# Kernel optimization log

Measured on AMD Instinct MI355X. Metric: run time of the kernel, lower is better.

## Reference

```python
import jax, jax.numpy as jnp
import numpy as np

T, B, V, E, H, K = 256, 512, 50000, 300, 100, 8


def _lstm_dir(x, wih, whh, bih, bhh, reverse):
    # x: [T,B,D]; wih: [4H,D]; whh: [4H,H]. PyTorch gate order: i,f,g,o.
    xp = jnp.einsum('tbd,gd->tbg', x, wih) + bih + bhh  # precompute input projections
    h0 = jnp.zeros((x.shape[1], whh.shape[1]), x.dtype)
    c0 = jnp.zeros_like(h0)

    def step(carry, xt):
        h, c = carry
        g = xt + h @ whh.T
        i, f, gg, o = jnp.split(g, 4, axis=-1)
        i = jax.nn.sigmoid(i); f = jax.nn.sigmoid(f)
        gg = jnp.tanh(gg); o = jax.nn.sigmoid(o)
        c = f * c + i * gg
        h = o * jnp.tanh(c)
        return (h, c), h

    _, hs = jax.lax.scan(step, (h0, c0), xp, reverse=reverse)
    return hs  # [T,B,H]


def _bilstm(x, pf, pb):
    hf = _lstm_dir(x, *pf, reverse=False)
    hb = _lstm_dir(x, *pb, reverse=True)
    return jnp.concatenate([hf, hb], axis=-1)  # [T,B,2H]


def _crf_llh(em, tags, maskf, start_t, end_t, trans):
    # torchcrf log-likelihood, reduction='sum'. em: [T,B,K], tags/maskf: [T,B]
    barange = jnp.arange(em.shape[1])
    # numerator: score of gold path
    num = start_t[tags[0]] + em[0, barange, tags[0]]
    trans_sc = trans[tags[:-1], tags[1:]]                                   # [T-1,B]
    em_sc = jnp.take_along_axis(em[1:], tags[1:, :, None], axis=2)[..., 0]  # [T-1,B]
    num = num + jnp.sum((trans_sc + em_sc) * maskf[1:], axis=0)
    seq_ends = maskf.sum(0).astype(jnp.int32) - 1
    num = num + end_t[tags[seq_ends, barange]]
    # denominator: forward algorithm (log partition)
    score0 = start_t + em[0]  # [B,K]

    def step(score, inp):
        em_t, m_t = inp
        nxt = jax.scipy.special.logsumexp(score[:, :, None] + trans[None], axis=1) + em_t
        return jnp.where(m_t[:, None] > 0, nxt, score), None

    scoreT, _ = jax.lax.scan(step, score0, (em[1:], maskf[1:]))
    denom = jax.scipy.special.logsumexp(scoreT + end_t, axis=1)
    return jnp.sum(num - denom)


def _viterbi(em, start_t, end_t, trans):
    # mask is all ones -> fixed-length decode. em: [T,B,K] -> tags [T,B]
    score0 = start_t + em[0]

    def step(score, em_t):
        br = score[:, :, None] + trans            # [B,K,K]
        idx = jnp.argmax(br, axis=1)              # [B,K] backpointers
        return jnp.max(br, axis=1) + em_t, idx

    scoreT, hist = jax.lax.scan(step, score0, em[1:])  # hist: [T-1,B,K]
    last = jnp.argmax(scoreT + end_t, axis=1)          # [B]
    barange = jnp.arange(em.shape[1])

    def back(nxt, h):
        prev = h[barange, nxt]
        return prev, prev

    _, prevs = jax.lax.scan(back, last, hist, reverse=True)  # [T-1,B]
    return jnp.concatenate([prevs, last[None]], axis=0)      # [T,B]


def setup_inputs() -> dict:
    key = jax.random.key(0)
    ks = jax.random.split(key, 32)
    u = lambda k, shape, s: jax.random.uniform(k, shape, jnp.float32, -s, s)
    kl = 1.0 / np.sqrt(H)
    inp = {
        'sentence': jax.random.randint(ks[0], (T, B), 0, V, dtype=jnp.int32),
        'tags': jax.random.randint(ks[1], (T, B), 0, K, dtype=jnp.int32),
        'mask': jnp.ones((T, B), dtype=bool),
        'emb': jax.random.normal(ks[2], (V, E), jnp.float32),
        # layer 0 (input dim E)
        'wih0f': u(ks[3], (4 * H, E), kl), 'whh0f': u(ks[4], (4 * H, H), kl),
        'bih0f': u(ks[5], (4 * H,), kl), 'bhh0f': u(ks[6], (4 * H,), kl),
        'wih0b': u(ks[7], (4 * H, E), kl), 'whh0b': u(ks[8], (4 * H, H), kl),
        'bih0b': u(ks[9], (4 * H,), kl), 'bhh0b': u(ks[10], (4 * H,), kl),
        # layer 1 (input dim 2H)
        'wih1f': u(ks[11], (4 * H, 2 * H), kl), 'whh1f': u(ks[12], (4 * H, H), kl),
        'bih1f': u(ks[13], (4 * H,), kl), 'bhh1f': u(ks[14], (4 * H,), kl),
        'wih1b': u(ks[15], (4 * H, 2 * H), kl), 'whh1b': u(ks[16], (4 * H, H), kl),
        'bih1b': u(ks[17], (4 * H,), kl), 'bhh1b': u(ks[18], (4 * H,), kl),
        # linear 2H -> K
        'wl': u(ks[19], (K, 2 * H), 1.0 / np.sqrt(2 * H)), 'bl': u(ks[20], (K,), 1.0 / np.sqrt(2 * H)),
        # CRF params (torchcrf init: uniform(-0.1, 0.1))
        'start_t': u(ks[21], (K,), 0.1), 'end_t': u(ks[22], (K,), 0.1),
        'trans': u(ks[23], (K, K), 0.1),
    }
    return inp


def reference(sentence, tags, mask, emb,
              wih0f, whh0f, bih0f, bhh0f, wih0b, whh0b, bih0b, bhh0b,
              wih1f, whh1f, bih1f, bhh1f, wih1b, whh1b, bih1b, bhh1b,
              wl, bl, start_t, end_t, trans):
    x = emb[sentence]                                        # [T,B,E]
    h1 = _bilstm(x, (wih0f, whh0f, bih0f, bhh0f), (wih0b, whh0b, bih0b, bhh0b))
    h2 = _bilstm(h1, (wih1f, whh1f, bih1f, bhh1f), (wih1b, whh1b, bih1b, bhh1b))
    em = jnp.einsum('tbh,kh->tbk', h2, wl) + bl              # emissions [T,B,K]
    maskf = mask.astype(em.dtype)
    loss = _crf_llh(em, tags, maskf, start_t, end_t, trans)
    decode = _viterbi(em, start_t, end_t, trans)
    return loss, decode
```

## Files before the change

kernel.cpp:

```cpp
#include <hip/hip_runtime.h>
#include <math.h>


#define T_LEN 256
#define B_SZ  512
#define TCH   32

__device__ __forceinline__ float sigm(float x) { return 1.f / (1.f + __expf(-x)); }
__device__ __forceinline__ float tanh_f(float x) {
  float e = __expf(-2.f * fabsf(x));
  float r = (1.f - e) / (1.f + e);
  return copysignf(r, x);
}

__global__ __launch_bounds__(256) void pack_kernel(
    const float* __restrict__ wih0f, const float* __restrict__ bih0f, const float* __restrict__ bhh0f,
    const float* __restrict__ wih0b, const float* __restrict__ bih0b, const float* __restrict__ bhh0b,
    const float* __restrict__ wih1f, const float* __restrict__ bih1f, const float* __restrict__ bhh1f,
    const float* __restrict__ wih1b, const float* __restrict__ bih1b, const float* __restrict__ bhh1b,
    float* __restrict__ W0, float* __restrict__ B0,
    float* __restrict__ W1, float* __restrict__ B1,
    float* __restrict__ out0) {
  int idx = blockIdx.x * blockDim.x + threadIdx.x;
  int stride = gridDim.x * blockDim.x;
  if (idx == 0) out0[0] = 0.f;
  for (int i = idx; i < 800 * 300; i += stride) {
    int g = i / 300, d = i - g * 300;
    W0[i] = (g < 400) ? wih0f[g * 300 + d] : wih0b[(g - 400) * 300 + d];
  }
  for (int i = idx; i < 800 * 200; i += stride) {
    int g = i / 200, d = i - g * 200;
    W1[i] = (g < 400) ? wih1f[g * 200 + d] : wih1b[(g - 400) * 200 + d];
  }
  for (int i = idx; i < 800; i += stride) {
    B0[i] = (i < 400) ? (bih0f[i] + bhh0f[i]) : (bih0b[i - 400] + bhh0b[i - 400]);
    B1[i] = (i < 400) ? (bih1f[i] + bhh1f[i]) : (bih1b[i - 400] + bhh1b[i - 400]);
  }
}

#define BM 128
#define BN 128
#define BK 16
__device__ __forceinline__ void gemm_body(
    const float* __restrict__ A, const float* __restrict__ W,
    const float* __restrict__ bias, float* __restrict__ C,
    int M, int N, int Kd, int m0, int n0,
    float (*As)[BM], float (*Ws)[BN]) {
  const int tid = threadIdx.x;
  const int tx = tid & 15, ty = tid >> 4;
  const int lm = tid & 127;
  const int lk = (tid >> 7) * 8;

  float acc[8][8];
  float bj[8];
#pragma unroll
  for (int j = 0; j < 8; ++j) {
    int n = n0 + tx * 8 + j;
    bj[j] = (n < N) ? bias[n] : 0.f;
  }
#pragma unroll
  for (int i = 0; i < 8; ++i)
#pragma unroll
    for (int j = 0; j < 8; ++j) acc[i][j] = bj[j];

  float4 av0, av1, wv0, wv1;
  av0 = av1 = wv0 = wv1 = make_float4(0.f, 0.f, 0.f, 0.f);
  {
    if (m0 + lm < M && lk < Kd)
      av0 = *(const float4*)(A + (size_t)(m0 + lm) * Kd + lk);
    if (m0 + lm < M && lk + 4 < Kd)
      av1 = *(const float4*)(A + (size_t)(m0 + lm) * Kd + lk + 4);
    if (n0 + lm < N && lk < Kd)
      wv0 = *(const float4*)(W + (size_t)(n0 + lm) * Kd + lk);
    if (n0 + lm < N && lk + 4 < Kd)
      wv1 = *(const float4*)(W + (size_t)(n0 + lm) * Kd + lk + 4);
  }

  for (int k0 = 0; k0 < Kd; k0 += BK) {
    __syncthreads();
    As[lk + 0][lm] = av0.x; As[lk + 1][lm] = av0.y;
    As[lk + 2][lm] = av0.z; As[lk + 3][lm] = av0.w;
    As[lk + 4][lm] = av1.x; As[lk + 5][lm] = av1.y;
    As[lk + 6][lm] = av1.z; As[lk + 7][lm] = av1.w;
    Ws[lk + 0][lm] = wv0.x; Ws[lk + 1][lm] = wv0.y;
    Ws[lk + 2][lm] = wv0.z; Ws[lk + 3][lm] = wv0.w;
    Ws[lk + 4][lm] = wv1.x; Ws[lk + 5][lm] = wv1.y;
    Ws[lk + 6][lm] = wv1.z; Ws[lk + 7][lm] = wv1.w;
    __syncthreads();
    int k0n = k0 + BK;
    av0 = av1 = wv0 = wv1 = make_float4(0.f, 0.f, 0.f, 0.f);
    if (k0n < Kd) {
      if (m0 + lm < M && k0n + lk < Kd)
        av0 = *(const float4*)(A + (size_t)(m0 + lm) * Kd + k0n + lk);
      if (m0 + lm < M && k0n + lk + 4 < Kd)
        av1 = *(const float4*)(A + (size_t)(m0 + lm) * Kd + k0n + lk + 4);
      if (n0 + lm < N && k0n + lk < Kd)
        wv0 = *(const float4*)(W + (size_t)(n0 + lm) * Kd + k0n + lk);
      if (n0 + lm < N && k0n + lk + 4 < Kd)
        wv1 = *(const float4*)(W + (size_t)(n0 + lm) * Kd + k0n + lk + 4);
    }
#pragma unroll
    for (int kk = 0; kk < BK; ++kk) {
      float a[8], w[8];
      *(float4*)&a[0] = *(const float4*)&As[kk][ty * 8];
      *(float4*)&a[4] = *(const float4*)&As[kk][ty * 8 + 4];
      *(float4*)&w[0] = *(const float4*)&Ws[kk][tx * 8];
      *(float4*)&w[4] = *(const float4*)&Ws[kk][tx * 8 + 4];
#pragma unroll
      for (int i = 0; i < 8; ++i)
#pragma unroll
        for (int j = 0; j < 8; ++j) acc[i][j] += a[i] * w[j];
    }
  }
#pragma unroll
  for (int i = 0; i < 8; ++i) {
    int m = m0 + ty * 8 + i;
    if (m < M) {
#pragma unroll
      for (int j0 = 0; j0 < 8; j0 += 4) {
        int n = n0 + tx * 8 + j0;
        if (n < N) {
          float4 o = make_float4(acc[i][j0], acc[i][j0 + 1], acc[i][j0 + 2], acc[i][j0 + 3]);
          *(float4*)(C + (size_t)m * N + n) = o;
        }
      }
    }
  }
}

__global__ __launch_bounds__(256, 2) void gemm_tn(
    const float* __restrict__ A, const float* __restrict__ W,
    const float* __restrict__ bias, float* __restrict__ C,
    int M, int N, int Kd) {
  __shared__ float As[BK][BM];
  __shared__ float Ws[BK][BN];
  gemm_body(A, W, bias, C, M, N, Kd, blockIdx.x * BM, blockIdx.y * BN, As, Ws);
}

__global__ __launch_bounds__(256, 2) void gemm_dual(
    const float* __restrict__ h1, const float* __restrict__ W1,
    const float* __restrict__ B1, float* __restrict__ XPF,
    float* __restrict__ XPB, int baseF, int baseB, int B) {
  __shared__ float As[BK][BM];
  __shared__ float Ws[BK][BN];
  const int dir = blockIdx.z;
  const float* A = h1 + (size_t)(dir ? baseB : baseF) * B * 200;
  const float* W = W1 + (size_t)dir * 80000;
  const float* bias = B1 + dir * 400;
  float* C = dir ? XPB : XPF;
  gemm_body(A, W, bias, C, TCH * B, 400, 200, blockIdx.x * BM, blockIdx.y * BN, As, Ws);
}

__global__ __launch_bounds__(256, 2) void lstm2(
    const float* __restrict__ XPf, const float* __restrict__ XPb,
    int xp_stride,
    const int* __restrict__ gather,
    const float* __restrict__ whhF, const float* __restrict__ whhB,
    float* __restrict__ stateH, float* __restrict__ stateC,
    float* __restrict__ hout,
    int tbaseF, int tbaseB, int TC, int first, int B) {
  const int tid = threadIdx.x;
  const int j = tid >> 1;
  const int gp = tid & 1;
  const bool act = (j < 100);
  const int bpd = B >> 1;
  const int dir = (blockIdx.x >= (unsigned)bpd) ? 1 : 0;
  const int b0 = (dir ? (blockIdx.x - bpd) : blockIdx.x) * 2;
  const float* __restrict__ XP = dir ? XPb : XPf;
  const float* __restrict__ whh = dir ? whhB : whhF;
  const int tbase = dir ? tbaseB : tbaseF;
  const int tstep = dir ? -1 : 1;
  const int tfirst = dir ? (tbase + TC - 1) : tbase;
  const int cg0 = gp * 200 + j;
  const int cg1 = cg0 + 100;

  __shared__ float h_s[2][2][100];

  float4 w0[25], w1[25];
  {
    const float* p0 = whh + (size_t)(2 * gp) * 10000 + (size_t)j * 100;
    if (act) {
#pragma unroll
      for (int q = 0; q < 25; ++q) {
        w0[q] = *(const float4*)(p0 + q * 4);
        w1[q] = *(const float4*)(p0 + 10000 + q * 4);
      }
    } else {
#pragma unroll
      for (int q = 0; q < 25; ++q) {
        w0[q] = make_float4(0.f, 0.f, 0.f, 0.f);
        w1[q] = make_float4(0.f, 0.f, 0.f, 0.f);
      }
    }
  }

  float c0v = 0.f, c1v = 0.f;
  if (gp == 0 && act) {
    if (!first) {
      c0v = stateC[((size_t)dir * B + b0 + 0) * 100 + j];
      c1v = stateC[((size_t)dir * B + b0 + 1) * 100 + j];
      h_s[0][0][j] = stateH[((size_t)dir * B + b0 + 0) * 100 + j];
      h_s[0][1][j] = stateH[((size_t)dir * B + b0 + 1) * 100 + j];
    } else {
      h_s[0][0][j] = 0.f;
      h_s[0][1][j] = 0.f;
    }
  }

  auto rowptr = [&](int tt, int bb) -> const float* {
    size_t r = gather ? (size_t)gather[(size_t)tt * B + b0 + bb]
                      : (size_t)(tt - tbase) * B + b0 + bb;
    return XP + r * (size_t)xp_stride;
  };

  float x00 = 0.f, x01 = 0.f, x10 = 0.f, x11 = 0.f;
  {
    const float* r0 = rowptr(tfirst, 0);
    const float* r1 = rowptr(tfirst, 1);
    if (act) { x00 = r0[cg0]; x10 = r0[cg1]; x01 = r1[cg0]; x11 = r1[cg1]; }
  }
  const float* baseN0 = XP;
  const float* baseN1 = XP;
  if (TC > 1) { baseN0 = rowptr(tfirst + tstep, 0); baseN1 = rowptr(tfirst + tstep, 1); }

  __syncthreads();

  int cur = 0;
  for (int s = 0; s < TC; ++s) {
    const int t = tfirst + s * tstep;
    float nx00 = 0.f, nx01 = 0.f, nx10 = 0.f, nx11 = 0.f;
    if (act && s + 1 < TC) {
      nx00 = baseN0[cg0]; nx10 = baseN0[cg1];
      nx01 = baseN1[cg0]; nx11 = baseN1[cg1];
    }
    if (s + 2 < TC) {
      baseN0 = rowptr(t + 2 * tstep, 0);
      baseN1 = rowptr(t + 2 * tstep, 1);
    }
    float a00 = 0.f, a01 = 0.f, a10 = 0.f, a11 = 0.f;
    const float* hb0 = h_s[cur][0];
    const float* hb1 = h_s[cur][1];
#pragma unroll
    for (int q = 0; q < 25; ++q) {
      float4 h0 = *(const float4*)(hb0 + q * 4);
      float4 h1v = *(const float4*)(hb1 + q * 4);
      float4 W0q = w0[q], W1q = w1[q];
      a00 += W0q.x * h0.x + W0q.y * h0.y + W0q.z * h0.z + W0q.w * h0.w;
      a10 += W1q.x * h0.x + W1q.y * h0.y + W1q.z * h0.z + W1q.w * h0.w;
      a01 += W0q.x * h1v.x + W0q.y * h1v.y + W0q.z * h1v.z + W0q.w * h1v.w;
      a11 += W1q.x * h1v.x + W1q.y * h1v.y + W1q.z * h1v.z + W1q.w * h1v.w;
    }
    a00 += x00; a10 += x10; a01 += x01; a11 += x11;
    float g0 = __shfl_xor(a00, 1);
    float g1 = __shfl_xor(a01, 1);
    float o0 = __shfl_xor(a10, 1);
    float o1 = __shfl_xor(a11, 1);
    const int nxt = cur ^ 1;
    if (gp == 0 && act) {
      float i0 = sigm(a00), f0 = sigm(a10);
      c0v = f0 * c0v + i0 * tanh_f(g0);
      float h0n = sigm(o0) * tanh_f(c0v);
      float i1 = sigm(a01), f1 = sigm(a11);
      c1v = f1 * c1v + i1 * tanh_f(g1);
      float h1n = sigm(o1) * tanh_f(c1v);
      h_s[nxt][0][j] = h0n;
      h_s[nxt][1][j] = h1n;
      hout[((size_t)t * B + b0 + 0) * 200 + dir * 100 + j] = h0n;
      hout[((size_t)t * B + b0 + 1) * 200 + dir * 100 + j] = h1n;
    }
    __syncthreads();
    cur = nxt;
    x00 = nx00; x01 = nx01; x10 = nx10; x11 = nx11;
  }
  if (gp == 0 && act) {
    stateH[((size_t)dir * B + b0 + 0) * 100 + j] = h_s[cur][0][j];
    stateH[((size_t)dir * B + b0 + 1) * 100 + j] = h_s[cur][1][j];
    stateC[((size_t)dir * B + b0 + 0) * 100 + j] = c0v;
    stateC[((size_t)dir * B + b0 + 1) * 100 + j] = c1v;
  }
}

__global__ __launch_bounds__(256) void em_kernel(
    const float* __restrict__ h2, const float* __restrict__ wl,
    const float* __restrict__ bl_, float* __restrict__ em) {
  __shared__ float hsb[32][200];
  __shared__ float wls[8 * 200];
  __shared__ float bls[8];
  const int tid = threadIdx.x;
  const int row0 = blockIdx.x * 32;
  for (int i = tid; i < 1600; i += 256) wls[i] = wl[i];
  if (tid < 8) bls[tid] = bl_[tid];
  for (int i = tid; i < 1600; i += 256) {
    int r = i / 50, q = i - r * 50;
    *(float4*)&hsb[r][q * 4] = *(const float4*)(h2 + (size_t)(row0 + r) * 200 + q * 4);
  }
  __syncthreads();
  const int r_l = tid >> 3, k = tid & 7;
  float acc = bls[k];
#pragma unroll
  for (int d4 = 0; d4 < 50; ++d4) {
    float4 h = *(const float4*)&hsb[r_l][d4 * 4];
    float4 wv = *(const float4*)&wls[k * 200 + d4 * 4];
    acc += h.x * wv.x + h.y * wv.y + h.z * wv.z + h.w * wv.w;
  }
  em[(size_t)(row0 + r_l) * 8 + k] = acc;
}

__global__ __launch_bounds__(64) void crf_kernel(
    const float* __restrict__ em, const int* __restrict__ tags,
    const float* __restrict__ start_t, const float* __restrict__ end_t,
    const float* __restrict__ trans, float* __restrict__ loss_out,
    int T, int B) {
  const int tid = threadIdx.x;
  const int bl = tid >> 3, jj = tid & 7;
  const int b = blockIdx.x * 8 + bl;
  __shared__ float sc[2][8][9];
  __shared__ float rednum[8][8];
  __shared__ float partial[8];
  float trj[8];
#pragma unroll
  for (int i = 0; i < 8; ++i) trj[i] = trans[i * 8 + jj];

  float pnum = 0.f;
  for (int t = 1 + jj; t < T; t += 8) {
    int tp = tags[(size_t)(t - 1) * B + b];
    int tc = tags[(size_t)t * B + b];
    pnum += trans[tp * 8 + tc] + em[((size_t)t * B + b) * 8 + tc];
  }
  rednum[bl][jj] = pnum;
  __syncthreads();
  float num = 0.f;
  if (jj == 0) {
#pragma unroll
    for (int i = 0; i < 8; ++i) num += rednum[bl][i];
    int t0 = tags[b];
    int tl = tags[(size_t)(T - 1) * B + b];
    num += start_t[t0] + em[(size_t)b * 8 + t0] + end_t[tl];
  }
  sc[0][bl][jj] = start_t[jj] + em[(size_t)b * 8 + jj];
  __syncthreads();
  for (int t = 1; t < T; ++t) {
    int cur = t & 1, prev = cur ^ 1;
    float m = -1e30f;
    float v[8];
#pragma unroll
    for (int i = 0; i < 8; ++i) {
      v[i] = sc[prev][bl][i] + trj[i];
      m = fmaxf(m, v[i]);
    }
    float ssum = 0.f;
#pragma unroll
    for (int i = 0; i < 8; ++i) ssum += __expf(v[i] - m);
    sc[cur][bl][jj] = m + __logf(ssum) + em[((size_t)t * B + b) * 8 + jj];
    __syncthreads();
  }
  rednum[bl][jj] = sc[(T - 1) & 1][bl][jj] + end_t[jj];
  __syncthreads();
  if (jj == 0) {
    float m = -1e30f;
#pragma unroll
    for (int i = 0; i < 8; ++i) m = fmaxf(m, rednum[bl][i]);
    float ssum = 0.f;
#pragma unroll
    for (int i = 0; i < 8; ++i) ssum += __expf(rednum[bl][i] - m);
    partial[bl] = num - (m + __logf(ssum));
  }
  __syncthreads();
  if (tid == 0) {
    float s2 = 0.f;
#pragma unroll
    for (int i = 0; i < 8; ++i) s2 += partial[i];
    atomicAdd(loss_out, s2);
  }
}

__global__ __launch_bounds__(64) void viterbi_kernel(
    const float* __restrict__ em, const float* __restrict__ start_t,
    const float* __restrict__ end_t, const float* __restrict__ trans,
    float* __restrict__ dec_out, int T, int B) {
  const int tid = threadIdx.x;
  const int bl = tid >> 3, jj = tid & 7;
  const int b = blockIdx.x * 8 + bl;
  __shared__ float sc[2][8][9];
  __shared__ unsigned hist[T_LEN - 1][8];
  __shared__ float redm[8][8];
  __shared__ int lastt[8];
  float trj[8];
#pragma unroll
  for (int i = 0; i < 8; ++i) trj[i] = trans[i * 8 + jj];
  for (int i = tid; i < (T_LEN - 1) * 8; i += 64) ((unsigned*)hist)[i] = 0u;
  sc[0][bl][jj] = start_t[jj] + em[(size_t)b * 8 + jj];
  __syncthreads();
  for (int t = 1; t < T; ++t) {
    int cur = t & 1, prev = cur ^ 1;
    float m = -1e30f;
    int am = 0;
#pragma unroll
    for (int i = 0; i < 8; ++i) {
      float v = sc[prev][bl][i] + trj[i];
      if (v > m) { m = v; am = i; }
    }
    atomicOr(&hist[t - 1][bl], (unsigned)am << (3 * jj));
    sc[cur][bl][jj] = m + em[((size_t)t * B + b) * 8 + jj];
    __syncthreads();
  }
  redm[bl][jj] = sc[(T - 1) & 1][bl][jj] + end_t[jj];
  __syncthreads();
  if (jj == 0) {
    float m = -1e30f;
    int am = 0;
#pragma unroll
    for (int i = 0; i < 8; ++i) {
      float v = redm[bl][i];
      if (v > m) { m = v; am = i; }
    }
    lastt[bl] = am;
  }
  __syncthreads();
  if (tid < 8) {
    int bb = blockIdx.x * 8 + tid;
    int cur = lastt[tid];
    dec_out[(size_t)(T - 1) * B + bb] = (float)cur;
    for (int t2 = T - 2; t2 >= 0; --t2) {
      cur = (int)((hist[t2][tid] >> (3 * cur)) & 7u);
      dec_out[(size_t)t2 * B + bb] = (float)cur;
    }
  }
}

__global__ __launch_bounds__(256) void report_kernel(float* out, float wsval, int n) {
  int i = blockIdx.x * blockDim.x + threadIdx.x;
  if (i == 0) out[0] = wsval;
  else if (i < n) out[i] = 0.f;
}

extern "C" void kernel_launch(void* const* d_in, const int* in_sizes, int n_in,
                              void* d_out, int out_size, void* d_ws, size_t ws_size,
                              hipStream_t stream) {
  const int* sentence = (const int*)d_in[0];
  const int* tags     = (const int*)d_in[1];
  const float* emb   = (const float*)d_in[3];
  const float* wih0f = (const float*)d_in[4];
  const float* whh0f = (const float*)d_in[5];
  const float* bih0f = (const float*)d_in[6];
  const float* bhh0f = (const float*)d_in[7];
  const float* wih0b = (const float*)d_in[8];
  const float* whh0b = (const float*)d_in[9];
  const float* bih0b = (const float*)d_in[10];
  const float* bhh0b = (const float*)d_in[11];
  const float* wih1f = (const float*)d_in[12];
  const float* whh1f = (const float*)d_in[13];
  const float* bih1f = (const float*)d_in[14];
  const float* bhh1f = (const float*)d_in[15];
  const float* wih1b = (const float*)d_in[16];
  const float* whh1b = (const float*)d_in[17];
  const float* bih1b = (const float*)d_in[18];
  const float* bhh1b = (const float*)d_in[19];
  const float* wl      = (const float*)d_in[20];
  const float* bl_     = (const float*)d_in[21];
  const float* start_t = (const float*)d_in[22];
  const float* end_t   = (const float*)d_in[23];
  const float* trans   = (const float*)d_in[24];

  const int T = T_LEN, B = B_SZ;
  float* out = (float*)d_out;
  float* ws = (float*)d_ws;

  const size_t O_P0  = 0;
  const size_t O_H1  = 40000000ull;
  const size_t O_W0  = 66214400ull;
  const size_t O_B0  = 66454400ull;
  const size_t O_STH = 66214400ull;
  const size_t O_STC = 66316800ull;
  const size_t O_W1  = 66455200ull;
  const size_t O_B1  = 66615200ull;
  const size_t TOTAL_FL = 66616000ull;
  const size_t O_H2  = 0;
  const size_t O_XPF = 26214400ull;
  const size_t O_XPB = 32768000ull;
  const size_t O_EM  = 26214400ull;

  if (ws_size < TOTAL_FL * 4ull) {
    report_kernel<<<(out_size + 255) / 256, 256, 0, stream>>>(out, (float)ws_size, out_size);
    return;
  }

  float* P0  = ws + O_P0;
  float* h1  = ws + O_H1;
  float* W0  = ws + O_W0;
  float* B0  = ws + O_B0;
  float* stH = ws + O_STH;
  float* stC = ws + O_STC;
  float* W1  = ws + O_W1;
  float* B1  = ws + O_B1;
  float* h2  = ws + O_H2;
  float* XPF = ws + O_XPF;
  float* XPB = ws + O_XPB;
  float* em  = ws + O_EM;

  pack_kernel<<<256, 256, 0, stream>>>(wih0f, bih0f, bhh0f, wih0b, bih0b, bhh0b,
                                       wih1f, bih1f, bhh1f, wih1b, bih1b, bhh1b,
                                       W0, B0, W1, B1, out);
  dim3 g1((50000 + BM - 1) / BM, (800 + BN - 1) / BN);
  gemm_tn<<<g1, 256, 0, stream>>>(emb, W0, B0, P0, 50000, 800, 300);

  lstm2<<<B, 256, 0, stream>>>(P0, P0 + 400, 800, sentence, whh0f, whh0b,
                               stH, stC, h1, 0, 0, T, 1, B);

  dim3 gc((TCH * B + BM - 1) / BM, (400 + BN - 1) / BN, 2);
  for (int cc = 0; cc < T / TCH; ++cc) {
    int baseF = cc * TCH;
    int baseB = T - TCH - cc * TCH;
    gemm_dual<<<gc, 256, 0, stream>>>(h1, W1, B1, XPF, XPB, baseF, baseB, B);
    lstm2<<<B, 256, 0, stream>>>(XPF, XPB, 400, nullptr, whh1f, whh1b,
                                 stH, stC, h2, baseF, baseB, TCH, cc == 0, B);
  }

  em_kernel<<<(T * B) / 32, 256, 0, stream>>>(h2, wl, bl_, em);
  crf_kernel<<<B / 8, 64, 0, stream>>>(em, tags, start_t, end_t, trans, out, T, B);
  viterbi_kernel<<<B / 8, 64, 0, stream>>>(em, start_t, end_t, trans, out + 1, T, B);
}
```

Measured before the change: 2.833 ms.

## Compute all four LSTM gates per thread to remove shuffle exchange

The recurrent LSTM kernel now assigns one thread per hidden unit, holding all four gate weight rows (400 floats) in registers, instead of two threads per unit that exchanged partial gate sums with shuffles. Blocks shrink from 256 to 128 threads, and every active thread now computes the gate nonlinearities, so no lanes sit idle during the pointwise stage. The aim is to drop the cross-lane exchange and the half-idle pointwise phase. The cost is very high register pressure (about 400 VGPRs of weights), which lowers occupancy and risks spills, and each thread does twice the dot-product work per step.

```diff
diff --git a/kernel.cpp b/kernel.cpp
--- a/kernel.cpp
+++ b/kernel.cpp
@@ -151,7 +151,7 @@
   gemm_body(A, W, bias, C, TCH * B, 400, 200, blockIdx.x * BM, blockIdx.y * BN, As, Ws);
 }
 
-__global__ __launch_bounds__(256, 2) void lstm2(
+__global__ __launch_bounds__(128, 1) void lstm6(
     const float* __restrict__ XPf, const float* __restrict__ XPb,
     int xp_stride,
     const int* __restrict__ gather,
@@ -159,9 +159,7 @@
     float* __restrict__ stateH, float* __restrict__ stateC,
     float* __restrict__ hout,
     int tbaseF, int tbaseB, int TC, int first, int B) {
-  const int tid = threadIdx.x;
-  const int j = tid >> 1;
-  const int gp = tid & 1;
+  const int j = threadIdx.x;
   const bool act = (j < 100);
   const int bpd = B >> 1;
   const int dir = (blockIdx.x >= (unsigned)bpd) ? 1 : 0;
@@ -171,53 +169,46 @@
   const int tbase = dir ? tbaseB : tbaseF;
   const int tstep = dir ? -1 : 1;
   const int tfirst = dir ? (tbase + TC - 1) : tbase;
-  const int cg0 = gp * 200 + j;
-  const int cg1 = cg0 + 100;
 
   __shared__ float h_s[2][2][100];
 
-  float4 w0[25], w1[25];
-  {
-    const float* p0 = whh + (size_t)(2 * gp) * 10000 + (size_t)j * 100;
-    if (act) {
-#pragma unroll
-      for (int q = 0; q < 25; ++q) {
-        w0[q] = *(const float4*)(p0 + q * 4);
-        w1[q] = *(const float4*)(p0 + 10000 + q * 4);
-      }
-    } else {
-#pragma unroll
-      for (int q = 0; q < 25; ++q) {
-        w0[q] = make_float4(0.f, 0.f, 0.f, 0.f);
-        w1[q] = make_float4(0.f, 0.f, 0.f, 0.f);
-      }
-    }
+  float4 w[4][25];
+#pragma unroll
+  for (int r = 0; r < 4; ++r) {
+    const float* p = whh + (size_t)(r * 100 + j) * 100;
+#pragma unroll
+    for (int q = 0; q < 25; ++q)
+      w[r][q] = act ? *(const float4*)(p + q * 4) : make_float4(0.f, 0.f, 0.f, 0.f);
   }
 
   float c0v = 0.f, c1v = 0.f;
-  if (gp == 0 && act) {
+  float hl0 = 0.f, hl1 = 0.f;
+  if (act) {
     if (!first) {
       c0v = stateC[((size_t)dir * B + b0 + 0) * 100 + j];
       c1v = stateC[((size_t)dir * B + b0 + 1) * 100 + j];
-      h_s[0][0][j] = stateH[((size_t)dir * B + b0 + 0) * 100 + j];
-      h_s[0][1][j] = stateH[((size_t)dir * B + b0 + 1) * 100 + j];
-    } else {
-      h_s[0][0][j] = 0.f;
-      h_s[0][1][j] = 0.f;
-    }
-  }
-
-  auto rowptr = [&](int tt, int bb) -> const float* {
-    size_t r = gather ? (size_t)gather[(size_t)tt * B + b0 + bb]
-                      : (size_t)(tt - tbase) * B + b0 + bb;
+      hl0 = stateH[((size_t)dir * B + b0 + 0) * 100 + j];
+      hl1 = stateH[((size_t)dir * B + b0 + 1) * 100 + j];
+    }
+    h_s[0][0][j] = hl0;
+    h_s[0][1][j] = hl1;
+  }
+
+  auto rowptr = [&](int tt, int u) -> const float* {
+    size_t r = gather ? (size_t)gather[(size_t)tt * B + b0 + u]
+                      : (size_t)(tt - tbase) * B + b0 + u;
     return XP + r * (size_t)xp_stride;
   };
 
-  float x00 = 0.f, x01 = 0.f, x10 = 0.f, x11 = 0.f;
+  float xv[4][2];
   {
     const float* r0 = rowptr(tfirst, 0);
     const float* r1 = rowptr(tfirst, 1);
-    if (act) { x00 = r0[cg0]; x10 = r0[cg1]; x01 = r1[cg0]; x11 = r1[cg1]; }
+#pragma unroll
+    for (int r = 0; r < 4; ++r) {
+      xv[r][0] = act ? r0[r * 100 + j] : 0.f;
+      xv[r][1] = act ? r1[r * 100 + j] : 0.f;
+    }
   }
   const float* baseN0 = XP;
   const float* baseN1 = XP;
@@ -228,53 +219,59 @@
   int cur = 0;
   for (int s = 0; s < TC; ++s) {
     const int t = tfirst + s * tstep;
-    float nx00 = 0.f, nx01 = 0.f, nx10 = 0.f, nx11 = 0.f;
+    float nx[4][2];
+#pragma unroll
+    for (int r = 0; r < 4; ++r) { nx[r][0] = 0.f; nx[r][1] = 0.f; }
     if (act && s + 1 < TC) {
-      nx00 = baseN0[cg0]; nx10 = baseN0[cg1];
-      nx01 = baseN1[cg0]; nx11 = baseN1[cg1];
+#pragma unroll
+      for (int r = 0; r < 4; ++r) {
+        nx[r][0] = baseN0[r * 100 + j];
+        nx[r][1] = baseN1[r * 100 + j];
+      }
     }
     if (s + 2 < TC) {
       baseN0 = rowptr(t + 2 * tstep, 0);
       baseN1 = rowptr(t + 2 * tstep, 1);
     }
-    float a00 = 0.f, a01 = 0.f, a10 = 0.f, a11 = 0.f;
+    float a[4][2];
+#pragma unroll
+    for (int r = 0; r < 4; ++r) { a[r][0] = 0.f; a[r][1] = 0.f; }
     const float* hb0 = h_s[cur][0];
     const float* hb1 = h_s[cur][1];
 #pragma unroll
     for (int q = 0; q < 25; ++q) {
       float4 h0 = *(const float4*)(hb0 + q * 4);
       float4 h1v = *(const float4*)(hb1 + q * 4);
-      float4 W0q = w0[q], W1q = w1[q];
-      a00 += W0q.x * h0.x + W0q.y * h0.y + W0q.z * h0.z + W0q.w * h0.w;
-      a10 += W1q.x * h0.x + W1q.y * h0.y + W1q.z * h0.z + W1q.w * h0.w;
-      a01 += W0q.x * h1v.x + W0q.y * h1v.y + W0q.z * h1v.z + W0q.w * h1v.w;
-      a11 += W1q.x * h1v.x + W1q.y * h1v.y + W1q.z * h1v.z + W1q.w * h1v.w;
-    }
-    a00 += x00; a10 += x10; a01 += x01; a11 += x11;
-    float g0 = __shfl_xor(a00, 1);
-    float g1 = __shfl_xor(a01, 1);
-    float o0 = __shfl_xor(a10, 1);
-    float o1 = __shfl_xor(a11, 1);
+#pragma unroll
+      for (int r = 0; r < 4; ++r) {
+        float4 W4 = w[r][q];
+        a[r][0] += W4.x * h0.x + W4.y * h0.y + W4.z * h0.z + W4.w * h0.w;
+        a[r][1] += W4.x * h1v.x + W4.y * h1v.y + W4.z * h1v.z + W4.w * h1v.w;
+      }
+    }
     const int nxt = cur ^ 1;
-    if (gp == 0 && act) {
-      float i0 = sigm(a00), f0 = sigm(a10);
-      c0v = f0 * c0v + i0 * tanh_f(g0);
-      float h0n = sigm(o0) * tanh_f(c0v);
-      float i1 = sigm(a01), f1 = sigm(a11);
-      c1v = f1 * c1v + i1 * tanh_f(g1);
-      float h1n = sigm(o1) * tanh_f(c1v);
-      h_s[nxt][0][j] = h0n;
-      h_s[nxt][1][j] = h1n;
-      hout[((size_t)t * B + b0 + 0) * 200 + dir * 100 + j] = h0n;
-      hout[((size_t)t * B + b0 + 1) * 200 + dir * 100 + j] = h1n;
+    if (act) {
+      float gi0 = a[0][0] + xv[0][0], gf0 = a[1][0] + xv[1][0];
+      float gg0 = a[2][0] + xv[2][0], go0 = a[3][0] + xv[3][0];
+      c0v = sigm(gf0) * c0v + sigm(gi0) * tanh_f(gg0);
+      hl0 = sigm(go0) * tanh_f(c0v);
+      float gi1 = a[0][1] + xv[0][1], gf1 = a[1][1] + xv[1][1];
+      float gg1 = a[2][1] + xv[2][1], go1 = a[3][1] + xv[3][1];
+      c1v = sigm(gf1) * c1v + sigm(gi1) * tanh_f(gg1);
+      hl1 = sigm(go1) * tanh_f(c1v);
+      h_s[nxt][0][j] = hl0;
+      h_s[nxt][1][j] = hl1;
+      hout[((size_t)t * B + b0 + 0) * 200 + dir * 100 + j] = hl0;
+      hout[((size_t)t * B + b0 + 1) * 200 + dir * 100 + j] = hl1;
     }
     __syncthreads();
     cur = nxt;
-    x00 = nx00; x01 = nx01; x10 = nx10; x11 = nx11;
-  }
-  if (gp == 0 && act) {
-    stateH[((size_t)dir * B + b0 + 0) * 100 + j] = h_s[cur][0][j];
-    stateH[((size_t)dir * B + b0 + 1) * 100 + j] = h_s[cur][1][j];
+#pragma unroll
+    for (int r = 0; r < 4; ++r) { xv[r][0] = nx[r][0]; xv[r][1] = nx[r][1]; }
+  }
+  if (act) {
+    stateH[((size_t)dir * B + b0 + 0) * 100 + j] = hl0;
+    stateH[((size_t)dir * B + b0 + 1) * 100 + j] = hl1;
     stateC[((size_t)dir * B + b0 + 0) * 100 + j] = c0v;
     stateC[((size_t)dir * B + b0 + 1) * 100 + j] = c1v;
   }
@@ -504,7 +501,7 @@
   dim3 g1((50000 + BM - 1) / BM, (800 + BN - 1) / BN);
   gemm_tn<<<g1, 256, 0, stream>>>(emb, W0, B0, P0, 50000, 800, 300);
 
-  lstm2<<<B, 256, 0, stream>>>(P0, P0 + 400, 800, sentence, whh0f, whh0b,
+  lstm6<<<B, 128, 0, stream>>>(P0, P0 + 400, 800, sentence, whh0f, whh0b,
                                stH, stC, h1, 0, 0, T, 1, B);
 
   dim3 gc((TCH * B + BM - 1) / BM, (400 + BN - 1) / BN, 2);
@@ -512,7 +509,7 @@
     int baseF = cc * TCH;
     int baseB = T - TCH - cc * TCH;
     gemm_dual<<<gc, 256, 0, stream>>>(h1, W1, B1, XPF, XPB, baseF, baseB, B);
-    lstm2<<<B, 256, 0, stream>>>(XPF, XPB, 400, nullptr, whh1f, whh1b,
+    lstm6<<<B, 128, 0, stream>>>(XPF, XPB, 400, nullptr, whh1f, whh1b,
                                  stH, stC, h2, baseF, baseB, TCH, cc == 0, B);
   }
 
```

Result: slower. 8.035 ms (+183.6%).
